# Performance work log

Measured on AMD Instinct MI355X. Metric: run time of the kernel, lower is better.

The kernel has to match this reference:

```python
import jax, jax.numpy as jnp
import numpy as np

B, T, C, H = 8, 2048, 1024, 128

def setup_inputs() -> dict:
    key = jax.random.key(0)
    k1, k2, k3, k4 = jax.random.split(key, 4)
    scale = 0.02
    return {
        "x": jax.random.normal(k1, (B, T, C), dtype=jnp.float32),
        "Wq": jax.random.normal(k2, (C, H), dtype=jnp.float32) * scale,
        "Wk": jax.random.normal(k3, (C, H), dtype=jnp.float32) * scale,
        "Wv": jax.random.normal(k4, (C, H), dtype=jnp.float32) * scale,
    }

def reference(x, Wq, Wk, Wv):
    # Single causal attention head (dropout p=0.0 -> identity)
    q = jnp.einsum('btc,ch->bth', x, Wq)
    k = jnp.einsum('btc,ch->bth', x, Wk)
    v = jnp.einsum('btc,ch->bth', x, Wv)
    head_size = k.shape[-1]
    scores = jnp.einsum('bth,bsh->bts', q, k) / jnp.sqrt(jnp.asarray(head_size, q.dtype))  # [B,T,T]
    causal = jnp.tril(jnp.ones((scores.shape[1], scores.shape[2]), dtype=bool))
    scores = jnp.where(causal, scores, -jnp.inf)
    weights = jax.nn.softmax(scores, axis=-1)
    context = jnp.einsum('bts,bsh->bth', weights, v)  # [B,T,H]
    return context
```

## Files before the change

kernel.cpp:

```cpp
#include <hip/hip_runtime.h>

typedef __bf16 bf16x8 __attribute__((ext_vector_type(8)));
typedef float f32x4 __attribute__((ext_vector_type(4)));
typedef float fv4 __attribute__((ext_vector_type(4)));

#define B_ 8
#define T_ 2048
#define C_ 1024
#define H_ 128

__global__ __launch_bounds__(256) void prep_kernel(
    const float* __restrict__ Wq, const float* __restrict__ Wk,
    const float* __restrict__ Wv, __bf16* __restrict__ Wt)
{
  __shared__ __bf16 ldsT[128 * 136];
  const int tid = threadIdx.x;
  const int k0 = blockIdx.x * 128;
  const int wsel = blockIdx.y;
  const float* W = wsel == 0 ? Wq : (wsel == 1 ? Wk : Wv);
#pragma unroll
  for (int i = 0; i < 16; ++i) {
    int fidx = tid + 256 * i;
    int k = fidx >> 5, h4 = (fidx & 31) << 2;
    fv4 w = *(const fv4*)(W + (size_t)(k0 + k) * H_ + h4);
#pragma unroll
    for (int j = 0; j < 4; ++j) ldsT[(h4 + j) * 136 + k] = (__bf16)w[j];
  }
  __syncthreads();
#pragma unroll
  for (int i = 0; i < 8; ++i) {
    int sidx = tid + 256 * i;
    int h = sidx >> 4, c8 = (sidx & 15) << 3;
    *(bf16x8*)(Wt + (size_t)wsel * H_ * C_ + (size_t)h * C_ + k0 + c8) =
        *(const bf16x8*)&ldsT[h * 136 + c8];
  }
}

__global__ __launch_bounds__(256) void proj_kernel(
    const float* __restrict__ x, const __bf16* __restrict__ Wt,
    __bf16* __restrict__ Qw, __bf16* __restrict__ Kw, __bf16* __restrict__ Vtw)
{
  __shared__ __align__(16) __bf16 ldsA[32 * 40];
  __shared__ __align__(16) __bf16 ldsB[384 * 40];
  const int tid = threadIdx.x;
  const int wave = tid >> 6, lane = tid & 63;
  const int q4 = lane >> 4, l16 = lane & 15;
  const int bt0 = blockIdx.x * 32;

  const f32x4 zero4 = {0.f, 0.f, 0.f, 0.f};
  f32x4 acc[2][6];
#pragma unroll
  for (int mt = 0; mt < 2; ++mt)
#pragma unroll
    for (int nt = 0; nt < 6; ++nt) acc[mt][nt] = zero4;

  const int arow = tid >> 2, acol8 = (tid & 3) << 3;

  fv4 xa[2][2];
  bf16x8 wp[2][6];
#pragma unroll
  for (int slot = 0; slot < 2; ++slot) {
    const int kb = slot * 32;
    if (tid < 128) {
      const float* s = x + (size_t)(bt0 + arow) * C_ + kb + acol8;
      xa[slot][0] = *(const fv4*)s;
      xa[slot][1] = *(const fv4*)(s + 4);
    }
#pragma unroll
    for (int i = 0; i < 6; ++i) {
      int idx = tid + 256 * i;
      int col = idx >> 2, k8 = (idx & 3) << 3;
      wp[slot][i] = *(const bf16x8*)(Wt + (size_t)col * C_ + kb + k8);
    }
  }

  for (int c = 0; c < 32; ++c) {
    const int s = c & 1;
    if (tid < 128) {
      bf16x8 v;
#pragma unroll
      for (int j = 0; j < 4; ++j) { v[j] = (__bf16)xa[s][0][j]; v[4 + j] = (__bf16)xa[s][1][j]; }
      *(bf16x8*)&ldsA[arow * 40 + acol8] = v;
    }
#pragma unroll
    for (int i = 0; i < 6; ++i) {
      int idx = tid + 256 * i;
      int col = idx >> 2, k8 = (idx & 3) << 3;
      *(bf16x8*)&ldsB[col * 40 + k8] = wp[s][i];
    }
    __syncthreads();
    const int kn = (c + 2 < 32) ? (c + 2) * 32 : c * 32;
    if (tid < 128) {
      const float* sp = x + (size_t)(bt0 + arow) * C_ + kn + acol8;
      xa[s][0] = *(const fv4*)sp;
      xa[s][1] = *(const fv4*)(sp + 4);
    }
#pragma unroll
    for (int i = 0; i < 6; ++i) {
      int idx = tid + 256 * i;
      int col = idx >> 2, k8 = (idx & 3) << 3;
      wp[s][i] = *(const bf16x8*)(Wt + (size_t)col * C_ + kn + k8);
    }
    bf16x8 af[2];
#pragma unroll
    for (int mt = 0; mt < 2; ++mt)
      af[mt] = *(const bf16x8*)&ldsA[(mt * 16 + l16) * 40 + q4 * 8];
#pragma unroll
    for (int nt = 0; nt < 6; ++nt) {
      bf16x8 bf = *(const bf16x8*)&ldsB[(wave * 96 + nt * 16 + l16) * 40 + q4 * 8];
#pragma unroll
      for (int mt = 0; mt < 2; ++mt)
        acc[mt][nt] = __builtin_amdgcn_mfma_f32_16x16x32_bf16(af[mt], bf, acc[mt][nt], 0, 0, 0);
    }
    __syncthreads();
  }

  const int b = bt0 >> 11, t0 = bt0 & (T_ - 1);
#pragma unroll
  for (int mt = 0; mt < 2; ++mt)
#pragma unroll
    for (int nt = 0; nt < 6; ++nt) {
      int gcol = wave * 96 + nt * 16 + l16;
#pragma unroll
      for (int r = 0; r < 4; ++r) {
        int row = bt0 + mt * 16 + q4 * 4 + r;
        float v = acc[mt][nt][r];
        if (gcol < 128) Qw[(size_t)row * H_ + gcol] = (__bf16)v;
        else if (gcol < 256) Kw[(size_t)row * H_ + (gcol - 128)] = (__bf16)v;
        else {
          int tl = mt * 16 + q4 * 4 + r;
          ldsB[(gcol - 256) * 40 + tl] = (__bf16)v;
        }
      }
    }
  __syncthreads();
#pragma unroll
  for (int i = 0; i < 2; ++i) {
    int idx = tid + 256 * i;
    int h = idx >> 2, t8 = (idx & 3) << 3;
    *(bf16x8*)(Vtw + ((size_t)b * H_ + h) * T_ + t0 + t8) =
        *(const bf16x8*)&ldsB[h * 40 + t8];
  }
}

__global__ __launch_bounds__(256) void attn_split(
    const __bf16* __restrict__ Q, const __bf16* __restrict__ K,
    const __bf16* __restrict__ Vt, __bf16* __restrict__ PO,
    float* __restrict__ Pl, float* __restrict__ out)
{
  __shared__ __align__(16) __bf16 ldsK[64 * 136];
  __shared__ __align__(16) __bf16 ldsV[128 * 72];
  __shared__ __align__(16) __bf16 ldsP[4][16 * 72];
  const int tid = threadIdx.x;
  const int wave = tid >> 6, lane = tid & 63;
  const int q4 = lane >> 4, l16 = lane & 15;
  const int b = blockIdx.y;
  int rem = blockIdx.x, qb = 0;
  while (rem >= (qb >> 3) + 1) { rem -= (qb >> 3) + 1; ++qb; }
  const int c = rem;
  const int tstart = c << 3;
  const int tend = min(tstart + 8, qb + 1);
  const int nch = (qb >> 3) + 1;
  const int qw = qb * 64 + wave * 16;
  const __bf16* Qb = Q + (size_t)b * T_ * H_;
  const __bf16* Kb = K + (size_t)b * T_ * H_;
  const __bf16* Vb = Vt + (size_t)b * H_ * T_;
  __bf16* ldsPw = &ldsP[wave][0];

  bf16x8 qf[4];
#pragma unroll
  for (int kc = 0; kc < 4; ++kc)
    qf[kc] = *(const bf16x8*)(Qb + (size_t)(qw + l16) * H_ + kc * 32 + q4 * 8);

  const f32x4 zero4 = {0.f, 0.f, 0.f, 0.f};
  f32x4 o[8];
#pragma unroll
  for (int nt = 0; nt < 8; ++nt) o[nt] = zero4;
  float lsum[4] = {0.f, 0.f, 0.f, 0.f};

  bf16x8 kp[4], vp[4];
#pragma unroll
  for (int i = 0; i < 4; ++i) {
    int idx = tid + 256 * i;
    int krow = idx >> 4, kcol8 = (idx & 15) << 3;
    kp[i] = *(const bf16x8*)(Kb + (size_t)(tstart * 64 + krow) * H_ + kcol8);
    int vrow = idx >> 3, vcol8 = (idx & 7) << 3;
    vp[i] = *(const bf16x8*)(Vb + (size_t)vrow * T_ + tstart * 64 + vcol8);
  }

  for (int t = tstart; t < tend; ++t) {
    const int kv0 = t << 6;
#pragma unroll
    for (int i = 0; i < 4; ++i) {
      int idx = tid + 256 * i;
      int krow = idx >> 4, kcol8 = (idx & 15) << 3;
      *(bf16x8*)&ldsK[krow * 136 + kcol8] = kp[i];
      int vrow = idx >> 3, vcol8 = (idx & 7) << 3;
      *(bf16x8*)&ldsV[vrow * 72 + vcol8] = vp[i];
    }
    __syncthreads();
    const int kvn = (t + 1 < tend) ? (kv0 + 64) : kv0;
#pragma unroll
    for (int i = 0; i < 4; ++i) {
      int idx = tid + 256 * i;
      int krow = idx >> 4, kcol8 = (idx & 15) << 3;
      kp[i] = *(const bf16x8*)(Kb + (size_t)(kvn + krow) * H_ + kcol8);
      int vrow = idx >> 3, vcol8 = (idx & 7) << 3;
      vp[i] = *(const bf16x8*)(Vb + (size_t)vrow * T_ + kvn + vcol8);
    }

    f32x4 s[4];
#pragma unroll
    for (int nt = 0; nt < 4; ++nt) s[nt] = zero4;
#pragma unroll
    for (int nt = 0; nt < 4; ++nt)
#pragma unroll
      for (int kc = 0; kc < 4; ++kc) {
        bf16x8 kf = *(const bf16x8*)&ldsK[(nt * 16 + l16) * 136 + kc * 32 + q4 * 8];
        s[nt] = __builtin_amdgcn_mfma_f32_16x16x32_bf16(qf[kc], kf, s[nt], 0, 0, 0);
      }

    if (t == qb) {
#pragma unroll
      for (int r = 0; r < 4; ++r) {
        const int grow = qw + q4 * 4 + r;
#pragma unroll
        for (int nt = 0; nt < 4; ++nt) {
          int col = kv0 + nt * 16 + l16;
          float p = (col <= grow) ? __expf(s[nt][r] * 0.08838834764831845f) : 0.f;
          lsum[r] += p;
          ldsPw[(q4 * 4 + r) * 72 + nt * 16 + l16] = (__bf16)p;
        }
      }
    } else {
#pragma unroll
      for (int r = 0; r < 4; ++r)
#pragma unroll
        for (int nt = 0; nt < 4; ++nt) {
          float p = __expf(s[nt][r] * 0.08838834764831845f);
          lsum[r] += p;
          ldsPw[(q4 * 4 + r) * 72 + nt * 16 + l16] = (__bf16)p;
        }
    }
#pragma unroll
    for (int kc2 = 0; kc2 < 2; ++kc2) {
      bf16x8 pf = *(const bf16x8*)&ldsPw[l16 * 72 + kc2 * 32 + q4 * 8];
#pragma unroll
      for (int nt = 0; nt < 8; ++nt) {
        bf16x8 vf = *(const bf16x8*)&ldsV[(nt * 16 + l16) * 72 + kc2 * 32 + q4 * 8];
        o[nt] = __builtin_amdgcn_mfma_f32_16x16x32_bf16(pf, vf, o[nt], 0, 0, 0);
      }
    }
    __syncthreads();
  }

  float lred[4];
#pragma unroll
  for (int r = 0; r < 4; ++r) {
    float l = lsum[r];
    l += __shfl_xor(l, 1);
    l += __shfl_xor(l, 2);
    l += __shfl_xor(l, 4);
    l += __shfl_xor(l, 8);
    lred[r] = l;
  }

  if (nch == 1) {
#pragma unroll
    for (int r = 0; r < 4; ++r) lred[r] = 1.f / lred[r];
#pragma unroll
    for (int nt = 0; nt < 8; ++nt)
#pragma unroll
      for (int r = 0; r < 4; ++r) {
        int row = qw + q4 * 4 + r;
        out[((size_t)b * T_ + row) * H_ + nt * 16 + l16] = o[nt][r] * lred[r];
      }
  } else {
    const int slot = b * 80 + qb + max(qb - 8, 0) + max(qb - 16, 0) + max(qb - 24, 0) + c;
    __bf16* POs = PO + (size_t)slot * 8192;
#pragma unroll
    for (int nt = 0; nt < 8; ++nt)
#pragma unroll
      for (int r = 0; r < 4; ++r)
        POs[(wave * 16 + q4 * 4 + r) * 128 + nt * 16 + l16] = (__bf16)o[nt][r];
    if (l16 == 0)
#pragma unroll
      for (int r = 0; r < 4; ++r)
        Pl[slot * 64 + wave * 16 + q4 * 4 + r] = lred[r];
  }
}

__global__ __launch_bounds__(256) void attn_combine(
    const __bf16* __restrict__ PO, const float* __restrict__ Pl,
    float* __restrict__ out)
{
  const int qb = 8 + (blockIdx.x >> 2);
  const int seg = blockIdx.x & 3;
  const int b = blockIdx.y;
  const int nch = (qb >> 3) + 1;
  const int slot0 = b * 80 + qb + max(qb - 8, 0) + max(qb - 16, 0) + max(qb - 24, 0);
  const int tid = threadIdx.x;
  const int rloc = seg * 16 + (tid >> 4);
  const int col8 = (tid & 15) << 3;
  float oacc[8] = {0.f};
  float lacc = 0.f;
  for (int cc = 0; cc < nch; ++cc) {
    const int slot = slot0 + cc;
    lacc += Pl[slot * 64 + rloc];
    bf16x8 v = *(const bf16x8*)(PO + (size_t)slot * 8192 + rloc * 128 + col8);
#pragma unroll
    for (int j = 0; j < 8; ++j) oacc[j] += (float)v[j];
  }
  const float inv = 1.f / lacc;
  float* op = out + ((size_t)b * T_ + qb * 64 + rloc) * H_ + col8;
  fv4 v0, v1;
#pragma unroll
  for (int j = 0; j < 4; ++j) { v0[j] = oacc[j] * inv; v1[j] = oacc[4 + j] * inv; }
  *(fv4*)op = v0;
  *(fv4*)(op + 4) = v1;
}

__global__ __launch_bounds__(256) void attn_mono(
    const __bf16* __restrict__ Q, const __bf16* __restrict__ K,
    const __bf16* __restrict__ Vt, float* __restrict__ out)
{
  __shared__ __align__(16) __bf16 ldsK[64 * 136];
  __shared__ __align__(16) __bf16 ldsV[128 * 72];
  __shared__ __align__(16) __bf16 ldsP[4][16 * 72];
  const int tid = threadIdx.x;
  const int wave = tid >> 6, lane = tid & 63;
  const int q4 = lane >> 4, l16 = lane & 15;
  const int qb = blockIdx.x, b = blockIdx.y;
  const int qw = qb * 64 + wave * 16;
  const __bf16* Qb = Q + (size_t)b * T_ * H_;
  const __bf16* Kb = K + (size_t)b * T_ * H_;
  const __bf16* Vb = Vt + (size_t)b * H_ * T_;
  __bf16* ldsPw = &ldsP[wave][0];

  bf16x8 qf[4];
#pragma unroll
  for (int kc = 0; kc < 4; ++kc)
    qf[kc] = *(const bf16x8*)(Qb + (size_t)(qw + l16) * H_ + kc * 32 + q4 * 8);

  const f32x4 zero4 = {0.f, 0.f, 0.f, 0.f};
  f32x4 o[8];
#pragma unroll
  for (int nt = 0; nt < 8; ++nt) o[nt] = zero4;
  float lsum[4] = {0.f, 0.f, 0.f, 0.f};
  const int ntile = qb + 1;

  bf16x8 kp[4], vp[4];
#pragma unroll
  for (int i = 0; i < 4; ++i) {
    int idx = tid + 256 * i;
    int krow = idx >> 4, kcol8 = (idx & 15) << 3;
    kp[i] = *(const bf16x8*)(Kb + (size_t)krow * H_ + kcol8);
    int vrow = idx >> 3, vcol8 = (idx & 7) << 3;
    vp[i] = *(const bf16x8*)(Vb + (size_t)vrow * T_ + vcol8);
  }

  for (int t = 0; t < ntile; ++t) {
    const int kv0 = t << 6;
#pragma unroll
    for (int i = 0; i < 4; ++i) {
      int idx = tid + 256 * i;
      int krow = idx >> 4, kcol8 = (idx & 15) << 3;
      *(bf16x8*)&ldsK[krow * 136 + kcol8] = kp[i];
      int vrow = idx >> 3, vcol8 = (idx & 7) << 3;
      *(bf16x8*)&ldsV[vrow * 72 + vcol8] = vp[i];
    }
    __syncthreads();
    int kvn = (t + 1 < ntile) ? (kv0 + 64) : kv0;
#pragma unroll
    for (int i = 0; i < 4; ++i) {
      int idx = tid + 256 * i;
      int krow = idx >> 4, kcol8 = (idx & 15) << 3;
      kp[i] = *(const bf16x8*)(Kb + (size_t)(kvn + krow) * H_ + kcol8);
      int vrow = idx >> 3, vcol8 = (idx & 7) << 3;
      vp[i] = *(const bf16x8*)(Vb + (size_t)vrow * T_ + kvn + vcol8);
    }
    f32x4 s[4];
#pragma unroll
    for (int nt = 0; nt < 4; ++nt) s[nt] = zero4;
#pragma unroll
    for (int nt = 0; nt < 4; ++nt)
#pragma unroll
      for (int kc = 0; kc < 4; ++kc) {
        bf16x8 kf = *(const bf16x8*)&ldsK[(nt * 16 + l16) * 136 + kc * 32 + q4 * 8];
        s[nt] = __builtin_amdgcn_mfma_f32_16x16x32_bf16(qf[kc], kf, s[nt], 0, 0, 0);
      }
#pragma unroll
    for (int r = 0; r < 4; ++r) {
      const int grow = qw + q4 * 4 + r;
#pragma unroll
      for (int nt = 0; nt < 4; ++nt) {
        int col = kv0 + nt * 16 + l16;
        float p = (col <= grow) ? __expf(s[nt][r] * 0.08838834764831845f) : 0.f;
        lsum[r] += p;
        ldsPw[(q4 * 4 + r) * 72 + nt * 16 + l16] = (__bf16)p;
      }
    }
#pragma unroll
    for (int kc2 = 0; kc2 < 2; ++kc2) {
      bf16x8 pf = *(const bf16x8*)&ldsPw[l16 * 72 + kc2 * 32 + q4 * 8];
#pragma unroll
      for (int nt = 0; nt < 8; ++nt) {
        bf16x8 vf = *(const bf16x8*)&ldsV[(nt * 16 + l16) * 72 + kc2 * 32 + q4 * 8];
        o[nt] = __builtin_amdgcn_mfma_f32_16x16x32_bf16(pf, vf, o[nt], 0, 0, 0);
      }
    }
    __syncthreads();
  }
  float rinv[4];
#pragma unroll
  for (int r = 0; r < 4; ++r) {
    float l = lsum[r];
    l += __shfl_xor(l, 1);
    l += __shfl_xor(l, 2);
    l += __shfl_xor(l, 4);
    l += __shfl_xor(l, 8);
    rinv[r] = 1.f / l;
  }
#pragma unroll
  for (int nt = 0; nt < 8; ++nt)
#pragma unroll
    for (int r = 0; r < 4; ++r) {
      int row = qw + q4 * 4 + r;
      out[((size_t)b * T_ + row) * H_ + nt * 16 + l16] = o[nt][r] * rinv[r];
    }
}

extern "C" void kernel_launch(void* const* d_in, const int* in_sizes, int n_in,
                              void* d_out, int out_size, void* d_ws, size_t ws_size,
                              hipStream_t stream) {
  const float* x  = (const float*)d_in[0];
  const float* Wq = (const float*)d_in[1];
  const float* Wk = (const float*)d_in[2];
  const float* Wv = (const float*)d_in[3];
  __bf16* ws = (__bf16*)d_ws;
  __bf16* Qw  = ws;
  __bf16* Kw  = ws + (size_t)B_ * T_ * H_;
  __bf16* Vtw = ws + (size_t)2 * B_ * T_ * H_;
  __bf16* Wt  = ws + (size_t)3 * B_ * T_ * H_;
  const size_t bf16_elems = 6684672;
  __bf16* PO = ws + bf16_elems;
  float* Pl = (float*)(ws + bf16_elems + (size_t)640 * 8192);
  const size_t need = bf16_elems * 2 + (size_t)640 * 8192 * 2 + (size_t)640 * 64 * 4;
  float* out = (float*)d_out;

  prep_kernel<<<dim3(8, 3), 256, 0, stream>>>(Wq, Wk, Wv, Wt);
  proj_kernel<<<512, 256, 0, stream>>>(x, Wt, Qw, Kw, Vtw);
  if (ws_size >= need) {
    attn_split<<<dim3(80, 8), 256, 0, stream>>>(Qw, Kw, Vtw, PO, Pl, out);
    attn_combine<<<dim3(96, 8), 256, 0, stream>>>(PO, Pl, out);
  } else {
    attn_mono<<<dim3(32, 8), 256, 0, stream>>>(Qw, Kw, Vtw, out);
  }
}
```

Baseline: 170.8 us.

## Load MFMA fragments directly from global memory, dropping LDS staging in projection and attention

The projection kernel and the split attention kernel now have each wave load its x/W and K/V MFMA operand fragments straight from global memory into registers, removing the LDS staging buffers and block-wide barriers. Launch bounds are raised to request two blocks per CU. The non-split attention kernel drops its register prefetch and loads K/V into LDS synchronously. The aim is to cut LDS traffic and sync overhead. In exchange, each wave of a block redundantly fetches the same K/V (or W) tiles from global/L2, uses uncoalesced 16-byte strided accesses, and loses load/compute overlap.

```diff
diff --git a/kernel.cpp b/kernel.cpp
--- a/kernel.cpp
+++ b/kernel.cpp
@@ -36,17 +36,20 @@
   }
 }
 
-__global__ __launch_bounds__(256) void proj_kernel(
+__global__ __launch_bounds__(256, 2) void proj_kernel(
     const float* __restrict__ x, const __bf16* __restrict__ Wt,
     __bf16* __restrict__ Qw, __bf16* __restrict__ Kw, __bf16* __restrict__ Vtw)
 {
-  __shared__ __align__(16) __bf16 ldsA[32 * 40];
-  __shared__ __align__(16) __bf16 ldsB[384 * 40];
+  __shared__ __align__(16) __bf16 ldsT[128 * 40];
   const int tid = threadIdx.x;
   const int wave = tid >> 6, lane = tid & 63;
   const int q4 = lane >> 4, l16 = lane & 15;
   const int bt0 = blockIdx.x * 32;
 
+  const float* xb0 = x + (size_t)(bt0 + l16) * C_ + q4 * 8;
+  const float* xb1 = xb0 + 16 * C_;
+  const __bf16* wb = Wt + (size_t)(wave * 96 + l16) * C_ + q4 * 8;
+
   const f32x4 zero4 = {0.f, 0.f, 0.f, 0.f};
   f32x4 acc[2][6];
 #pragma unroll
@@ -54,65 +57,46 @@
 #pragma unroll
     for (int nt = 0; nt < 6; ++nt) acc[mt][nt] = zero4;
 
-  const int arow = tid >> 2, acol8 = (tid & 3) << 3;
-
-  fv4 xa[2][2];
+  fv4 xa[2][2][2];
   bf16x8 wp[2][6];
 #pragma unroll
-  for (int slot = 0; slot < 2; ++slot) {
-    const int kb = slot * 32;
-    if (tid < 128) {
-      const float* s = x + (size_t)(bt0 + arow) * C_ + kb + acol8;
-      xa[slot][0] = *(const fv4*)s;
-      xa[slot][1] = *(const fv4*)(s + 4);
-    }
-#pragma unroll
-    for (int i = 0; i < 6; ++i) {
-      int idx = tid + 256 * i;
-      int col = idx >> 2, k8 = (idx & 3) << 3;
-      wp[slot][i] = *(const bf16x8*)(Wt + (size_t)col * C_ + kb + k8);
-    }
+  for (int s = 0; s < 2; ++s) {
+    const int kb = s * 32;
+    xa[s][0][0] = *(const fv4*)(xb0 + kb);
+    xa[s][0][1] = *(const fv4*)(xb0 + kb + 4);
+    xa[s][1][0] = *(const fv4*)(xb1 + kb);
+    xa[s][1][1] = *(const fv4*)(xb1 + kb + 4);
+#pragma unroll
+    for (int nt = 0; nt < 6; ++nt)
+      wp[s][nt] = *(const bf16x8*)(wb + (size_t)nt * 16 * C_ + kb);
   }
 
   for (int c = 0; c < 32; ++c) {
     const int s = c & 1;
-    if (tid < 128) {
-      bf16x8 v;
-#pragma unroll
-      for (int j = 0; j < 4; ++j) { v[j] = (__bf16)xa[s][0][j]; v[4 + j] = (__bf16)xa[s][1][j]; }
-      *(bf16x8*)&ldsA[arow * 40 + acol8] = v;
-    }
-#pragma unroll
-    for (int i = 0; i < 6; ++i) {
-      int idx = tid + 256 * i;
-      int col = idx >> 2, k8 = (idx & 3) << 3;
-      *(bf16x8*)&ldsB[col * 40 + k8] = wp[s][i];
-    }
-    __syncthreads();
+    bf16x8 af[2];
+#pragma unroll
+    for (int mt = 0; mt < 2; ++mt)
+#pragma unroll
+      for (int j = 0; j < 4; ++j) {
+        af[mt][j] = (__bf16)xa[s][mt][0][j];
+        af[mt][4 + j] = (__bf16)xa[s][mt][1][j];
+      }
+    bf16x8 bcur[6];
+#pragma unroll
+    for (int nt = 0; nt < 6; ++nt) bcur[nt] = wp[s][nt];
     const int kn = (c + 2 < 32) ? (c + 2) * 32 : c * 32;
-    if (tid < 128) {
-      const float* sp = x + (size_t)(bt0 + arow) * C_ + kn + acol8;
-      xa[s][0] = *(const fv4*)sp;
-      xa[s][1] = *(const fv4*)(sp + 4);
-    }
-#pragma unroll
-    for (int i = 0; i < 6; ++i) {
-      int idx = tid + 256 * i;
-      int col = idx >> 2, k8 = (idx & 3) << 3;
-      wp[s][i] = *(const bf16x8*)(Wt + (size_t)col * C_ + kn + k8);
-    }
-    bf16x8 af[2];
-#pragma unroll
-    for (int mt = 0; mt < 2; ++mt)
-      af[mt] = *(const bf16x8*)&ldsA[(mt * 16 + l16) * 40 + q4 * 8];
-#pragma unroll
-    for (int nt = 0; nt < 6; ++nt) {
-      bf16x8 bf = *(const bf16x8*)&ldsB[(wave * 96 + nt * 16 + l16) * 40 + q4 * 8];
+    xa[s][0][0] = *(const fv4*)(xb0 + kn);
+    xa[s][0][1] = *(const fv4*)(xb0 + kn + 4);
+    xa[s][1][0] = *(const fv4*)(xb1 + kn);
+    xa[s][1][1] = *(const fv4*)(xb1 + kn + 4);
+#pragma unroll
+    for (int nt = 0; nt < 6; ++nt)
+      wp[s][nt] = *(const bf16x8*)(wb + (size_t)nt * 16 * C_ + kn);
+#pragma unroll
+    for (int nt = 0; nt < 6; ++nt)
 #pragma unroll
       for (int mt = 0; mt < 2; ++mt)
-        acc[mt][nt] = __builtin_amdgcn_mfma_f32_16x16x32_bf16(af[mt], bf, acc[mt][nt], 0, 0, 0);
-    }
-    __syncthreads();
+        acc[mt][nt] = __builtin_amdgcn_mfma_f32_16x16x32_bf16(af[mt], bcur[nt], acc[mt][nt], 0, 0, 0);
   }
 
   const int b = bt0 >> 11, t0 = bt0 & (T_ - 1);
@@ -127,10 +111,7 @@
         float v = acc[mt][nt][r];
         if (gcol < 128) Qw[(size_t)row * H_ + gcol] = (__bf16)v;
         else if (gcol < 256) Kw[(size_t)row * H_ + (gcol - 128)] = (__bf16)v;
-        else {
-          int tl = mt * 16 + q4 * 4 + r;
-          ldsB[(gcol - 256) * 40 + tl] = (__bf16)v;
-        }
+        else ldsT[(gcol - 256) * 40 + (mt * 16 + q4 * 4 + r)] = (__bf16)v;
       }
     }
   __syncthreads();
@@ -139,17 +120,15 @@
     int idx = tid + 256 * i;
     int h = idx >> 2, t8 = (idx & 3) << 3;
     *(bf16x8*)(Vtw + ((size_t)b * H_ + h) * T_ + t0 + t8) =
-        *(const bf16x8*)&ldsB[h * 40 + t8];
-  }
-}
-
-__global__ __launch_bounds__(256) void attn_split(
+        *(const bf16x8*)&ldsT[h * 40 + t8];
+  }
+}
+
+__global__ __launch_bounds__(256, 2) void attn_split(
     const __bf16* __restrict__ Q, const __bf16* __restrict__ K,
     const __bf16* __restrict__ Vt, __bf16* __restrict__ PO,
     float* __restrict__ Pl, float* __restrict__ out)
 {
-  __shared__ __align__(16) __bf16 ldsK[64 * 136];
-  __shared__ __align__(16) __bf16 ldsV[128 * 72];
   __shared__ __align__(16) __bf16 ldsP[4][16 * 72];
   const int tid = threadIdx.x;
   const int wave = tid >> 6, lane = tid & 63;
@@ -178,36 +157,20 @@
   for (int nt = 0; nt < 8; ++nt) o[nt] = zero4;
   float lsum[4] = {0.f, 0.f, 0.f, 0.f};
 
-  bf16x8 kp[4], vp[4];
-#pragma unroll
-  for (int i = 0; i < 4; ++i) {
-    int idx = tid + 256 * i;
-    int krow = idx >> 4, kcol8 = (idx & 15) << 3;
-    kp[i] = *(const bf16x8*)(Kb + (size_t)(tstart * 64 + krow) * H_ + kcol8);
-    int vrow = idx >> 3, vcol8 = (idx & 7) << 3;
-    vp[i] = *(const bf16x8*)(Vb + (size_t)vrow * T_ + tstart * 64 + vcol8);
-  }
-
   for (int t = tstart; t < tend; ++t) {
     const int kv0 = t << 6;
-#pragma unroll
-    for (int i = 0; i < 4; ++i) {
-      int idx = tid + 256 * i;
-      int krow = idx >> 4, kcol8 = (idx & 15) << 3;
-      *(bf16x8*)&ldsK[krow * 136 + kcol8] = kp[i];
-      int vrow = idx >> 3, vcol8 = (idx & 7) << 3;
-      *(bf16x8*)&ldsV[vrow * 72 + vcol8] = vp[i];
-    }
-    __syncthreads();
-    const int kvn = (t + 1 < tend) ? (kv0 + 64) : kv0;
-#pragma unroll
-    for (int i = 0; i < 4; ++i) {
-      int idx = tid + 256 * i;
-      int krow = idx >> 4, kcol8 = (idx & 15) << 3;
-      kp[i] = *(const bf16x8*)(Kb + (size_t)(kvn + krow) * H_ + kcol8);
-      int vrow = idx >> 3, vcol8 = (idx & 7) << 3;
-      vp[i] = *(const bf16x8*)(Vb + (size_t)vrow * T_ + kvn + vcol8);
-    }
+    bf16x8 kf[4][4];
+#pragma unroll
+    for (int nt = 0; nt < 4; ++nt)
+#pragma unroll
+      for (int kc = 0; kc < 4; ++kc)
+        kf[nt][kc] = *(const bf16x8*)(Kb + (size_t)(kv0 + nt * 16 + l16) * H_ + kc * 32 + q4 * 8);
+    bf16x8 vf[8][2];
+#pragma unroll
+    for (int nt = 0; nt < 8; ++nt)
+#pragma unroll
+      for (int k2 = 0; k2 < 2; ++k2)
+        vf[nt][k2] = *(const bf16x8*)(Vb + (size_t)(nt * 16 + l16) * T_ + kv0 + k2 * 32 + q4 * 8);
 
     f32x4 s[4];
 #pragma unroll
@@ -215,10 +178,8 @@
 #pragma unroll
     for (int nt = 0; nt < 4; ++nt)
 #pragma unroll
-      for (int kc = 0; kc < 4; ++kc) {
-        bf16x8 kf = *(const bf16x8*)&ldsK[(nt * 16 + l16) * 136 + kc * 32 + q4 * 8];
-        s[nt] = __builtin_amdgcn_mfma_f32_16x16x32_bf16(qf[kc], kf, s[nt], 0, 0, 0);
-      }
+      for (int kc = 0; kc < 4; ++kc)
+        s[nt] = __builtin_amdgcn_mfma_f32_16x16x32_bf16(qf[kc], kf[nt][kc], s[nt], 0, 0, 0);
 
     if (t == qb) {
 #pragma unroll
@@ -243,15 +204,12 @@
         }
     }
 #pragma unroll
-    for (int kc2 = 0; kc2 < 2; ++kc2) {
-      bf16x8 pf = *(const bf16x8*)&ldsPw[l16 * 72 + kc2 * 32 + q4 * 8];
-#pragma unroll
-      for (int nt = 0; nt < 8; ++nt) {
-        bf16x8 vf = *(const bf16x8*)&ldsV[(nt * 16 + l16) * 72 + kc2 * 32 + q4 * 8];
-        o[nt] = __builtin_amdgcn_mfma_f32_16x16x32_bf16(pf, vf, o[nt], 0, 0, 0);
-      }
-    }
-    __syncthreads();
+    for (int k2 = 0; k2 < 2; ++k2) {
+      bf16x8 pf = *(const bf16x8*)&ldsPw[l16 * 72 + k2 * 32 + q4 * 8];
+#pragma unroll
+      for (int nt = 0; nt < 8; ++nt)
+        o[nt] = __builtin_amdgcn_mfma_f32_16x16x32_bf16(pf, vf[nt][k2], o[nt], 0, 0, 0);
+    }
   }
 
   float lred[4];
@@ -349,36 +307,19 @@
   float lsum[4] = {0.f, 0.f, 0.f, 0.f};
   const int ntile = qb + 1;
 
-  bf16x8 kp[4], vp[4];
-#pragma unroll
-  for (int i = 0; i < 4; ++i) {
-    int idx = tid + 256 * i;
-    int krow = idx >> 4, kcol8 = (idx & 15) << 3;
-    kp[i] = *(const bf16x8*)(Kb + (size_t)krow * H_ + kcol8);
-    int vrow = idx >> 3, vcol8 = (idx & 7) << 3;
-    vp[i] = *(const bf16x8*)(Vb + (size_t)vrow * T_ + vcol8);
-  }
-
   for (int t = 0; t < ntile; ++t) {
     const int kv0 = t << 6;
 #pragma unroll
     for (int i = 0; i < 4; ++i) {
       int idx = tid + 256 * i;
       int krow = idx >> 4, kcol8 = (idx & 15) << 3;
-      *(bf16x8*)&ldsK[krow * 136 + kcol8] = kp[i];
+      *(bf16x8*)&ldsK[krow * 136 + kcol8] =
+          *(const bf16x8*)(Kb + (size_t)(kv0 + krow) * H_ + kcol8);
       int vrow = idx >> 3, vcol8 = (idx & 7) << 3;
-      *(bf16x8*)&ldsV[vrow * 72 + vcol8] = vp[i];
+      *(bf16x8*)&ldsV[vrow * 72 + vcol8] =
+          *(const bf16x8*)(Vb + (size_t)vrow * T_ + kv0 + vcol8);
     }
     __syncthreads();
-    int kvn = (t + 1 < ntile) ? (kv0 + 64) : kv0;
-#pragma unroll
-    for (int i = 0; i < 4; ++i) {
-      int idx = tid + 256 * i;
-      int krow = idx >> 4, kcol8 = (idx & 15) << 3;
-      kp[i] = *(const bf16x8*)(Kb + (size_t)(kvn + krow) * H_ + kcol8);
-      int vrow = idx >> 3, vcol8 = (idx & 7) << 3;
-      vp[i] = *(const bf16x8*)(Vb + (size_t)vrow * T_ + kvn + vcol8);
-    }
     f32x4 s[4];
 #pragma unroll
     for (int nt = 0; nt < 4; ++nt) s[nt] = zero4;
@@ -401,11 +342,11 @@
       }
     }
 #pragma unroll
-    for (int kc2 = 0; kc2 < 2; ++kc2) {
-      bf16x8 pf = *(const bf16x8*)&ldsPw[l16 * 72 + kc2 * 32 + q4 * 8];
+    for (int k2 = 0; k2 < 2; ++k2) {
+      bf16x8 pf = *(const bf16x8*)&ldsPw[l16 * 72 + k2 * 32 + q4 * 8];
 #pragma unroll
       for (int nt = 0; nt < 8; ++nt) {
-        bf16x8 vf = *(const bf16x8*)&ldsV[(nt * 16 + l16) * 72 + kc2 * 32 + q4 * 8];
+        bf16x8 vf = *(const bf16x8*)&ldsV[(nt * 16 + l16) * 72 + k2 * 32 + q4 * 8];
         o[nt] = __builtin_amdgcn_mfma_f32_16x16x32_bf16(pf, vf, o[nt], 0, 0, 0);
       }
     }
```

New measurement: 423.6 us. 148% more time.
